# Performance work log

Measured on AMD Instinct MI355X. Metric: run time of the kernel, lower is better.

## Reference

```python
import jax, jax.numpy as jnp
import numpy as np

N = 100000      # num nodes
E = 1600000     # num edges (avg degree 16)
H = 128         # hidden_channels
A = 8           # edge_attr_dim
HID = 16        # edge-MLP hidden dim
DELTA_T = 0.1
LN_EPS = 1e-5


def _layer_norm(x, g, b):
    mu = jnp.mean(x, axis=-1, keepdims=True)
    var = jnp.mean((x - mu) ** 2, axis=-1, keepdims=True)
    return (x - mu) * jax.lax.rsqrt(var + LN_EPS) * g + b


def _edge_mlp(ea, w1, b1, w2, b2):
    # [E,A] -> [E,1] -> [E]
    return (jnp.tanh(ea @ w1 + b1) @ w2 + b2).reshape(-1)


def _spmm_diff(vals, row, col, M, n):
    # Sparse matrix S = diag(d) + off, off[col,row] = vals (scatter-add on duplicates),
    # d = segment_sum(vals, col) with zeros replaced by 1.  Returns S @ M.
    d = jax.ops.segment_sum(vals, col, num_segments=n)
    d = d + (d == 0).astype(vals.dtype)
    off = jax.ops.segment_sum(vals[:, None] * M[row], col, num_segments=n)
    return d[:, None] * M + off


def setup_inputs() -> dict:
    key = jax.random.key(0)
    ks = jax.random.split(key, 12)
    def xavier(k, shape):
        lim = float(np.sqrt(6.0 / (shape[0] + shape[1])))
        return jax.random.uniform(k, shape, jnp.float32, -lim, lim)
    return {
        "u": jax.random.normal(ks[0], (N, H), jnp.float32),
        "edge_index": jax.random.randint(ks[1], (2, E), 0, N, jnp.int64),
        "edge_attr": jax.random.normal(ks[2], (E, A), jnp.float32),
        "num_nodes": N,
        "mlpx_w1": xavier(ks[3], (A, HID)), "mlpx_b1": jnp.zeros((HID,), jnp.float32),
        "mlpx_w2": xavier(ks[4], (HID, 1)), "mlpx_b2": jnp.zeros((1,), jnp.float32),
        "mlpz_w1": xavier(ks[5], (A, HID)), "mlpz_b1": jnp.zeros((HID,), jnp.float32),
        "mlpz_w2": xavier(ks[6], (HID, 1)), "mlpz_b2": jnp.zeros((1,), jnp.float32),
        "weight": xavier(ks[7], (H, H)),
        "az_weight": xavier(ks[8], (H, H)),
        "norm1_g": jnp.ones((H,), jnp.float32), "norm1_b": jnp.zeros((H,), jnp.float32),
        "norm2_g": jnp.ones((H,), jnp.float32), "norm2_b": jnp.zeros((H,), jnp.float32),
        "delta_g": jnp.float32(0.5),
    }


def reference(u, edge_index, edge_attr, num_nodes,
              mlpx_w1, mlpx_b1, mlpx_w2, mlpx_b2,
              mlpz_w1, mlpz_b1, mlpz_w2, mlpz_b2,
              weight, az_weight, norm1_g, norm1_b, norm2_g, norm2_b, delta_g):
    row, col = edge_index[0], edge_index[1]
    delta_x = _edge_mlp(edge_attr, mlpx_w1, mlpx_b1, mlpx_w2, mlpx_b2) + 1e-6
    delta_z = _edge_mlp(edge_attr, mlpz_w1, mlpz_b1, mlpz_w2, mlpz_b2) + 1e-6

    uw2 = (u @ weight) ** 2
    first = _spmm_diff(1.0 / delta_x, row, col, uw2, num_nodes)
    first = jax.nn.silu(_layer_norm(first, norm1_g, norm1_b))

    azt = _spmm_diff(delta_z, row, col, u, num_nodes) @ az_weight
    azt = jax.nn.silu(_layer_norm(azt, norm2_g, norm2_b)) + 1e-6

    u_next = u - DELTA_T * (first + delta_g * azt)
    return jnp.clip(u_next, -10.0, 10.0)
```

## Files before the change

kernel.cpp:

```cpp
#include <hip/hip_runtime.h>

#define HH 128
#define LN_EPS 1e-5f

typedef _Float16 f16x8 __attribute__((ext_vector_type(8)));
typedef _Float16 f16x4 __attribute__((ext_vector_type(4)));
typedef float f32x4 __attribute__((ext_vector_type(4)));

__device__ __forceinline__ ushort f2bf(float v) {
    unsigned u = __float_as_uint(v);
    unsigned r = (u + 0x7FFFu + ((u >> 16) & 1u)) >> 16;
    return (ushort)r;
}
__device__ __forceinline__ float bf2f(unsigned lo16) { return __uint_as_float(lo16 << 16); }

__device__ __forceinline__ bool detect_i64(const int* __restrict__ ei) {
    int odd = ei[2 * (threadIdx.x & 63) + 1];
    return __ballot(odd == 0) == ~0ULL;
}

__global__ __launch_bounds__(256) void k_hist_rank(
    const int* __restrict__ ei, int* __restrict__ cnt,
    ushort* __restrict__ rank, int E)
{
    bool f64 = detect_i64(ei);
    int e0 = (blockIdx.x * 256 + threadIdx.x) * 4;
    if (e0 >= E) return;
    int c[4];
    int nv = min(4, E - e0);
    if (f64) {
        if (nv == 4) {
            int4 a = *(const int4*)&ei[2 * ((size_t)E + e0)];
            int4 b = *(const int4*)&ei[2 * ((size_t)E + e0) + 4];
            c[0] = a.x; c[1] = a.z; c[2] = b.x; c[3] = b.z;
        } else {
            for (int i = 0; i < nv; ++i) c[i] = ei[2 * ((size_t)E + e0 + i)];
        }
    } else {
        if (nv == 4) {
            int4 a = *(const int4*)&ei[(size_t)E + e0];
            c[0] = a.x; c[1] = a.y; c[2] = a.z; c[3] = a.w;
        } else {
            for (int i = 0; i < nv; ++i) c[i] = ei[(size_t)E + e0 + i];
        }
    }
    ushort rk[4];
    for (int i = 0; i < nv; ++i) rk[i] = (ushort)atomicAdd(&cnt[c[i]], 1);
    if (nv == 4) {
        *(ushort4*)&rank[e0] = make_ushort4(rk[0], rk[1], rk[2], rk[3]);
    } else {
        for (int i = 0; i < nv; ++i) rank[e0 + i] = rk[i];
    }
}

__global__ __launch_bounds__(256) void k_scan_a(
    const int* __restrict__ cnt, int* __restrict__ off,
    int* __restrict__ bs, int N)
{
    __shared__ int sm[256];
    int tid = threadIdx.x;
    int base = blockIdx.x * 1024 + tid * 4;
    int v0 = base + 0 < N ? cnt[base + 0] : 0;
    int v1 = base + 1 < N ? cnt[base + 1] : 0;
    int v2 = base + 2 < N ? cnt[base + 2] : 0;
    int v3 = base + 3 < N ? cnt[base + 3] : 0;
    int s = v0 + v1 + v2 + v3;
    sm[tid] = s;
    __syncthreads();
    for (int o = 1; o < 256; o <<= 1) {
        int t = (tid >= o) ? sm[tid - o] : 0;
        __syncthreads();
        sm[tid] += t;
        __syncthreads();
    }
    int excl = sm[tid] - s;
    if (tid == 255) bs[blockIdx.x] = sm[tid];
    if (base + 0 < N) off[base + 0] = excl;
    if (base + 1 < N) off[base + 1] = excl + v0;
    if (base + 2 < N) off[base + 2] = excl + v0 + v1;
    if (base + 3 < N) off[base + 3] = excl + v0 + v1 + v2;
}

__global__ __launch_bounds__(256) void k_scan_bc(
    int* __restrict__ off, const int* __restrict__ bs,
    int N, int E, int nb)
{
    __shared__ int sm[256];
    int tid = threadIdx.x;
    int s = tid < nb ? bs[tid] : 0;
    sm[tid] = s;
    __syncthreads();
    for (int o = 1; o < 256; o <<= 1) {
        int t = (tid >= o) ? sm[tid - o] : 0;
        __syncthreads();
        sm[tid] += t;
        __syncthreads();
    }
    int incl = sm[tid];
    __syncthreads();
    sm[tid] = incl - s;
    __syncthreads();
    int i = blockIdx.x * 256 + tid;
    if (i < N) off[i] += sm[i >> 10];
    if (i == 0) off[N] = E;
}

__global__ __launch_bounds__(256) void k_mlp_fill(
    const float* __restrict__ ea,
    const float* __restrict__ xw1, const float* __restrict__ xb1,
    const float* __restrict__ xw2, const float* __restrict__ xb2,
    const float* __restrict__ zw1, const float* __restrict__ zb1,
    const float* __restrict__ zw2, const float* __restrict__ zb2,
    const int* __restrict__ ei, const int* __restrict__ off,
    const ushort* __restrict__ rank, uint2* __restrict__ csr, int E)
{
    bool f64 = detect_i64(ei);
    int lane = threadIdx.x & 63;
    int wid  = threadIdx.x >> 6;
    int lr = lane & 15, lg = lane >> 4;

    f16x8 wxh, wxl, wzh, wzl;
#pragma unroll
    for (int k = 0; k < 8; ++k) {
        float wx = xw1[k * 16 + lr];
        float wz = zw1[k * 16 + lr];
        _Float16 xh = (_Float16)wx, zh = (_Float16)wz;
        _Float16 xl = (_Float16)(wx - (float)xh);
        _Float16 zl = (_Float16)(wz - (float)zh);
        bool zz = (lg != 0);
        wxh[k] = zz ? (_Float16)0.f : xh;
        wxl[k] = zz ? (_Float16)0.f : xl;
        wzh[k] = zz ? (_Float16)0.f : zh;
        wzl[k] = zz ? (_Float16)0.f : zl;
    }
    float b1x[4], b1z[4], w2x[4], w2z[4];
#pragma unroll
    for (int r = 0; r < 4; ++r) {
        int j = lg * 4 + r;
        b1x[r] = xb1[j]; b1z[r] = zb1[j];
        w2x[r] = xw2[j]; w2z[r] = zw2[j];
    }
    float bx2 = xb2[0], bz2 = zb2[0];

    long long base = (long long)blockIdx.x * 256 + wid * 64;
    long long eL = base + lane;
    size_t eld = (size_t)(eL < (long long)E ? eL : (long long)E - 1);
    float4 a0 = *(const float4*)&ea[eld * 8];
    float4 a1 = *(const float4*)&ea[eld * 8 + 4];
    float aa[8] = {a0.x, a0.y, a0.z, a0.w, a1.x, a1.y, a1.z, a1.w};
    f16x8 ah, al;
#pragma unroll
    for (int i = 0; i < 8; ++i) {
        _Float16 h = (_Float16)aa[i];
        ah[i] = h;
        al[i] = (_Float16)(aa[i] - (float)h);
    }
    uint4 avh = *reinterpret_cast<uint4*>(&ah);
    uint4 avl = *reinterpret_cast<uint4*>(&al);

#pragma unroll
    for (int g = 0; g < 4; ++g) {
        int src = g * 16 + lr;
        uint4 bvh, bvl;
        bvh.x = (unsigned)__shfl((int)avh.x, src);
        bvh.y = (unsigned)__shfl((int)avh.y, src);
        bvh.z = (unsigned)__shfl((int)avh.z, src);
        bvh.w = (unsigned)__shfl((int)avh.w, src);
        bvl.x = (unsigned)__shfl((int)avl.x, src);
        bvl.y = (unsigned)__shfl((int)avl.y, src);
        bvl.z = (unsigned)__shfl((int)avl.z, src);
        bvl.w = (unsigned)__shfl((int)avl.w, src);
        if (lg != 0) {
            bvh.x = 0; bvh.y = 0; bvh.z = 0; bvh.w = 0;
            bvl.x = 0; bvl.y = 0; bvl.z = 0; bvl.w = 0;
        }
        f16x8 bh = *reinterpret_cast<f16x8*>(&bvh);
        f16x8 bl = *reinterpret_cast<f16x8*>(&bvl);

        f32x4 dx = (f32x4){0.f, 0.f, 0.f, 0.f};
        f32x4 dz = (f32x4){0.f, 0.f, 0.f, 0.f};
        dx = __builtin_amdgcn_mfma_f32_16x16x32_f16(wxh, bh, dx, 0, 0, 0);
        dx = __builtin_amdgcn_mfma_f32_16x16x32_f16(wxh, bl, dx, 0, 0, 0);
        dx = __builtin_amdgcn_mfma_f32_16x16x32_f16(wxl, bh, dx, 0, 0, 0);
        dz = __builtin_amdgcn_mfma_f32_16x16x32_f16(wzh, bh, dz, 0, 0, 0);
        dz = __builtin_amdgcn_mfma_f32_16x16x32_f16(wzh, bl, dz, 0, 0, 0);
        dz = __builtin_amdgcn_mfma_f32_16x16x32_f16(wzl, bh, dz, 0, 0, 0);

        float sx = 0.f, sz = 0.f;
#pragma unroll
        for (int r = 0; r < 4; ++r) {
            float tx = __expf(2.f * (dx[r] + b1x[r]));
            float tz = __expf(2.f * (dz[r] + b1z[r]));
            sx += __fdividef(tx - 1.f, tx + 1.f) * w2x[r];
            sz += __fdividef(tz - 1.f, tz + 1.f) * w2z[r];
        }
        sx += __shfl_xor(sx, 16); sx += __shfl_xor(sx, 32);
        sz += __shfl_xor(sz, 16); sz += __shfl_xor(sz, 32);

        long long e = base + g * 16 + lane;
        if (lane < 16 && e < (long long)E) {
            int ec = (int)e;
            int r, c;
            if (f64) {
                r = ei[2 * (size_t)ec];
                c = ei[2 * ((size_t)E + ec)];
            } else {
                r = ei[ec];
                c = ei[(size_t)E + ec];
            }
            int p = off[c] + rank[ec];
            unsigned wx = f2bf(1.0f / (sx + bx2 + 1e-6f));
            unsigned wz = f2bf(sz + bz2 + 1e-6f);
            csr[p] = make_uint2((unsigned)r << 9, wx | (wz << 16));
        }
    }
}

#define WPITCH 136
__global__ __launch_bounds__(256) void k_gemm_fused(
    const float* __restrict__ A, const float* __restrict__ W0,
    const float* __restrict__ W1, _Float16* __restrict__ pk, int N)
{
    __shared__ _Float16 wt[256 * WPITCH];

    int tid = threadIdx.x;
    for (int it = 0; it < 8; ++it) {
        int tile = tid + it * 256;
        int k0 = (tile & 31) * 4, n0 = (tile >> 5) * 4;
        const float* src = (n0 < HH) ? W0 : W1;
        int cn = n0 & (HH - 1);
        float4 r0 = *(const float4*)&src[(k0 + 0) * HH + cn];
        float4 r1 = *(const float4*)&src[(k0 + 1) * HH + cn];
        float4 r2 = *(const float4*)&src[(k0 + 2) * HH + cn];
        float4 r3 = *(const float4*)&src[(k0 + 3) * HH + cn];
        const float* rr[4] = {(const float*)&r0, (const float*)&r1,
                              (const float*)&r2, (const float*)&r3};
#pragma unroll
        for (int j = 0; j < 4; ++j) {
            f16x4 v = {( _Float16)rr[0][j], (_Float16)rr[1][j],
                       ( _Float16)rr[2][j], (_Float16)rr[3][j]};
            *(f16x4*)&wt[(n0 + j) * WPITCH + k0] = v;
        }
    }
    __syncthreads();

    int w = tid >> 6, lane = tid & 63;
    int lr = lane & 15, lg = lane >> 4;

    f32x4 acc[2][16];
#pragma unroll
    for (int rt = 0; rt < 2; ++rt)
#pragma unroll
        for (int ct = 0; ct < 16; ++ct)
            acc[rt][ct] = (f32x4){0.f, 0.f, 0.f, 0.f};

    int rbase = blockIdx.x * 128 + w * 32 + lr;
    int ra0 = min(rbase,      N - 1);
    int ra1 = min(rbase + 16, N - 1);

    for (int ks = 0; ks < 4; ++ks) {
        int kofs = ks * 32 + lg * 8;
        f16x8 ufr[2];
#pragma unroll
        for (int rt = 0; rt < 2; ++rt) {
            const float* ap = &A[(size_t)(rt ? ra1 : ra0) * HH + kofs];
            float4 f0 = *(const float4*)ap;
            float4 f1 = *(const float4*)(ap + 4);
            f16x8 fr = {( _Float16)f0.x, (_Float16)f0.y, (_Float16)f0.z, (_Float16)f0.w,
                        ( _Float16)f1.x, (_Float16)f1.y, (_Float16)f1.z, (_Float16)f1.w};
            ufr[rt] = fr;
        }
#pragma unroll
        for (int ct = 0; ct < 16; ++ct) {
            f16x8 wfr = *(const f16x8*)&wt[(ct * 16 + lr) * WPITCH + kofs];
            acc[0][ct] = __builtin_amdgcn_mfma_f32_16x16x32_f16(wfr, ufr[0], acc[0][ct], 0, 0, 0);
            acc[1][ct] = __builtin_amdgcn_mfma_f32_16x16x32_f16(wfr, ufr[1], acc[1][ct], 0, 0, 0);
        }
    }

#pragma unroll
    for (int rt = 0; rt < 2; ++rt) {
        int r = blockIdx.x * 128 + w * 32 + rt * 16 + lr;
        if (r >= N) continue;
#pragma unroll
        for (int ct = 0; ct < 16; ++ct) {
            int c0 = ct * 16 + lg * 4;
            f16x4 o;
#pragma unroll
            for (int reg = 0; reg < 4; ++reg) {
                float v = acc[rt][ct][reg];
                if (ct < 8) v *= v;
                o[reg] = (_Float16)v;
            }
            *(f16x4*)&pk[(size_t)r * 256 + c0] = o;
        }
    }
}

__global__ __launch_bounds__(256) void k_gather(
    const uint2* __restrict__ csr, const int* __restrict__ off,
    const _Float16* __restrict__ pk, const float* __restrict__ u,
    const float* __restrict__ g1, const float* __restrict__ b1,
    const float* __restrict__ g2, const float* __restrict__ b2,
    const float* __restrict__ dgp, float* __restrict__ outp, int N)
{
    int wave = threadIdx.x >> 6, lane = threadIdx.x & 63;
    int node = blockIdx.x * 4 + wave;
    if (node >= N) return;
    int p = off[node], end = off[node + 1];

    const int  he   = lane >> 5;
    const int  sub  = lane & 31;
    const bool is_az = (lane & 16) != 0;
    const unsigned sub16 = (unsigned)sub * 16;
    const char* pkb = (const char*)pk;

    float acc[8];
#pragma unroll
    for (int j = 0; j < 8; ++j) acc[j] = 0.f;
    float dv = 0.f;

    while (p + 3 < end) {
        uint2 mA = csr[p + he];
        uint2 mB = csr[p + 2 + he];
        float wA = bf2f(is_az ? (mA.y >> 16) : (mA.y & 0xffffu));
        float wB = bf2f(is_az ? (mB.y >> 16) : (mB.y & 0xffffu));
        f16x8 qA = *(const f16x8*)(pkb + mA.x + sub16);
        f16x8 qB = *(const f16x8*)(pkb + mB.x + sub16);
#pragma unroll
        for (int j = 0; j < 8; ++j) acc[j] += wA * (float)qA[j];
#pragma unroll
        for (int j = 0; j < 8; ++j) acc[j] += wB * (float)qB[j];
        dv += wA + wB;
        p += 4;
    }
    while (p < end) {
        int idx = p + he;
        bool ok = idx < end;
        uint2 mm = csr[ok ? idx : p];
        float wv = bf2f(is_az ? (mm.y >> 16) : (mm.y & 0xffffu));
        if (!ok) wv = 0.f;
        f16x8 q = *(const f16x8*)(pkb + mm.x + sub16);
#pragma unroll
        for (int j = 0; j < 8; ++j) acc[j] += wv * (float)q[j];
        dv += wv;
        p += 2;
    }

#pragma unroll
    for (int j = 0; j < 8; ++j) acc[j] += __shfl_xor(acc[j], 32);
    dv += __shfl_xor(dv, 32);
    if (dv == 0.f) dv = 1.f;

    f16x8 qc = *(const f16x8*)(pkb + ((unsigned)node << 9) + sub16);
    float x[8];
#pragma unroll
    for (int j = 0; j < 8; ++j) x[j] = dv * (float)qc[j] + acc[j];

    float s = 0.f;
#pragma unroll
    for (int j = 0; j < 8; ++j) s += x[j];
    s += __shfl_xor(s, 1, 16); s += __shfl_xor(s, 2, 16);
    s += __shfl_xor(s, 4, 16); s += __shfl_xor(s, 8, 16);
    float mu = s * (1.f / 128.f);
    float s2 = 0.f;
#pragma unroll
    for (int j = 0; j < 8; ++j) { x[j] -= mu; s2 += x[j] * x[j]; }
    s2 += __shfl_xor(s2, 1, 16); s2 += __shfl_xor(s2, 2, 16);
    s2 += __shfl_xor(s2, 4, 16); s2 += __shfl_xor(s2, 8, 16);
    float rs = rsqrtf(s2 * (1.f / 128.f) + LN_EPS);

    int c8 = (sub & 15) * 8;
    const float* gp = is_az ? g2 : g1;
    const float* bp = is_az ? b2 : b1;
    float4 gv0 = *(const float4*)&gp[c8];
    float4 gv1 = *(const float4*)&gp[c8 + 4];
    float4 bv0 = *(const float4*)&bp[c8];
    float4 bv1 = *(const float4*)&bp[c8 + 4];
    float gA[8] = {gv0.x, gv0.y, gv0.z, gv0.w, gv1.x, gv1.y, gv1.z, gv1.w};
    float bA[8] = {bv0.x, bv0.y, bv0.z, bv0.w, bv1.x, bv1.y, bv1.z, bv1.w};

    float y[8];
#pragma unroll
    for (int j = 0; j < 8; ++j) {
        float v = x[j] * rs * gA[j] + bA[j];
        v = v / (1.f + __expf(-v));
        if (is_az) v += 1e-6f;
        y[j] = v;
    }

    float dg = *dgp;
    float yz[8];
#pragma unroll
    for (int j = 0; j < 8; ++j) yz[j] = __shfl_xor(y[j], 16);

    if (lane < 16) {
        size_t ub = (size_t)node * HH + c8;
        float4 u0 = *(const float4*)&u[ub];
        float4 u1 = *(const float4*)&u[ub + 4];
        float o[8];
        o[0] = u0.x; o[1] = u0.y; o[2] = u0.z; o[3] = u0.w;
        o[4] = u1.x; o[5] = u1.y; o[6] = u1.z; o[7] = u1.w;
#pragma unroll
        for (int j = 0; j < 8; ++j) {
            float v = o[j] - 0.1f * (y[j] + dg * yz[j]);
            o[j] = fminf(fmaxf(v, -10.f), 10.f);
        }
        *(float4*)&outp[ub]     = make_float4(o[0], o[1], o[2], o[3]);
        *(float4*)&outp[ub + 4] = make_float4(o[4], o[5], o[6], o[7]);
    }
}

extern "C" void kernel_launch(void* const* d_in, const int* in_sizes, int n_in,
                              void* d_out, int out_size, void* d_ws, size_t ws_size,
                              hipStream_t stream)
{
    const float* u   = (const float*)d_in[0];
    const int*   ei  = (const int*)d_in[1];
    const float* ea  = (const float*)d_in[2];
    const float* xw1 = (const float*)d_in[4];
    const float* xb1 = (const float*)d_in[5];
    const float* xw2 = (const float*)d_in[6];
    const float* xb2 = (const float*)d_in[7];
    const float* zw1 = (const float*)d_in[8];
    const float* zb1 = (const float*)d_in[9];
    const float* zw2 = (const float*)d_in[10];
    const float* zb2 = (const float*)d_in[11];
    const float* weight = (const float*)d_in[12];
    const float* azw = (const float*)d_in[13];
    const float* n1g = (const float*)d_in[14];
    const float* n1b = (const float*)d_in[15];
    const float* n2g = (const float*)d_in[16];
    const float* n2b = (const float*)d_in[17];
    const float* dgp = (const float*)d_in[18];

    int N = in_sizes[0] / HH;
    int E = in_sizes[2] / 8;

    _Float16* pk  = (_Float16*)d_ws;
    uint2* csr    = (uint2*)(pk + (size_t)N * 256);
    ushort* rank  = (ushort*)(csr + E);
    int* cnt      = (int*)(rank + ((E + 1) & ~1));
    int* off      = cnt + N;
    int* bs       = off + N + 1;

    (void)hipMemsetAsync(cnt, 0, (size_t)N * sizeof(int), stream);

    k_hist_rank<<<(E / 4 + 255) / 256, 256, 0, stream>>>(ei, cnt, rank, E);

    int nb = (N + 1023) / 1024;
    k_scan_a<<<nb, 256, 0, stream>>>(cnt, off, bs, N);
    k_scan_bc<<<(N + 255) / 256, 256, 0, stream>>>(off, bs, N, E, nb);

    k_mlp_fill<<<(E + 255) / 256, 256, 0, stream>>>(
        ea, xw1, xb1, xw2, xb2, zw1, zb1, zw2, zb2, ei, off, rank, csr, E);

    k_gemm_fused<<<(N + 127) / 128, 256, 0, stream>>>(u, weight, azw, pk, N);

    k_gather<<<(N + 3) / 4, 256, 0, stream>>>(
        csr, off, pk, u, n1g, n1b, n2g, n2b, dgp, (float*)d_out, N);
}
```

Baseline: 304.2 us.

## Merge GEMM and edge-MLP fill into one launch; unroll gather by eight

The dense GEMM blocks and the edge-MLP CSR-fill blocks now run as one kernel, split on block index, so the two independent phases overlap on the GPU and one launch is saved. The gather loop also gets an 8-edge unrolled step so more independent loads are in flight per iteration. The cost is that every block of the fused kernel reserves the ~68KB of shared memory the GEMM needs, which may lower occupancy for the fill blocks, and the extra unroll adds register pressure.

```diff
diff --git a/kernel.cpp b/kernel.cpp
--- a/kernel.cpp
+++ b/kernel.cpp
@@ -105,7 +105,10 @@
     if (i == 0) off[N] = E;
 }
 
-__global__ __launch_bounds__(256) void k_mlp_fill(
+#define WPITCH 136
+__global__ __launch_bounds__(256) void k_fat(
+    const float* __restrict__ A, const float* __restrict__ W0,
+    const float* __restrict__ W1, _Float16* __restrict__ pk, int N, int G,
     const float* __restrict__ ea,
     const float* __restrict__ xw1, const float* __restrict__ xb1,
     const float* __restrict__ xw2, const float* __restrict__ xb2,
@@ -114,185 +117,182 @@
     const int* __restrict__ ei, const int* __restrict__ off,
     const ushort* __restrict__ rank, uint2* __restrict__ csr, int E)
 {
-    bool f64 = detect_i64(ei);
-    int lane = threadIdx.x & 63;
-    int wid  = threadIdx.x >> 6;
-    int lr = lane & 15, lg = lane >> 4;
-
-    f16x8 wxh, wxl, wzh, wzl;
-#pragma unroll
-    for (int k = 0; k < 8; ++k) {
-        float wx = xw1[k * 16 + lr];
-        float wz = zw1[k * 16 + lr];
-        _Float16 xh = (_Float16)wx, zh = (_Float16)wz;
-        _Float16 xl = (_Float16)(wx - (float)xh);
-        _Float16 zl = (_Float16)(wz - (float)zh);
-        bool zz = (lg != 0);
-        wxh[k] = zz ? (_Float16)0.f : xh;
-        wxl[k] = zz ? (_Float16)0.f : xl;
-        wzh[k] = zz ? (_Float16)0.f : zh;
-        wzl[k] = zz ? (_Float16)0.f : zl;
-    }
-    float b1x[4], b1z[4], w2x[4], w2z[4];
-#pragma unroll
-    for (int r = 0; r < 4; ++r) {
-        int j = lg * 4 + r;
-        b1x[r] = xb1[j]; b1z[r] = zb1[j];
-        w2x[r] = xw2[j]; w2z[r] = zw2[j];
-    }
-    float bx2 = xb2[0], bz2 = zb2[0];
-
-    long long base = (long long)blockIdx.x * 256 + wid * 64;
-    long long eL = base + lane;
-    size_t eld = (size_t)(eL < (long long)E ? eL : (long long)E - 1);
-    float4 a0 = *(const float4*)&ea[eld * 8];
-    float4 a1 = *(const float4*)&ea[eld * 8 + 4];
-    float aa[8] = {a0.x, a0.y, a0.z, a0.w, a1.x, a1.y, a1.z, a1.w};
-    f16x8 ah, al;
-#pragma unroll
-    for (int i = 0; i < 8; ++i) {
-        _Float16 h = (_Float16)aa[i];
-        ah[i] = h;
-        al[i] = (_Float16)(aa[i] - (float)h);
-    }
-    uint4 avh = *reinterpret_cast<uint4*>(&ah);
-    uint4 avl = *reinterpret_cast<uint4*>(&al);
-
-#pragma unroll
-    for (int g = 0; g < 4; ++g) {
-        int src = g * 16 + lr;
-        uint4 bvh, bvl;
-        bvh.x = (unsigned)__shfl((int)avh.x, src);
-        bvh.y = (unsigned)__shfl((int)avh.y, src);
-        bvh.z = (unsigned)__shfl((int)avh.z, src);
-        bvh.w = (unsigned)__shfl((int)avh.w, src);
-        bvl.x = (unsigned)__shfl((int)avl.x, src);
-        bvl.y = (unsigned)__shfl((int)avl.y, src);
-        bvl.z = (unsigned)__shfl((int)avl.z, src);
-        bvl.w = (unsigned)__shfl((int)avl.w, src);
-        if (lg != 0) {
-            bvh.x = 0; bvh.y = 0; bvh.z = 0; bvh.w = 0;
-            bvl.x = 0; bvl.y = 0; bvl.z = 0; bvl.w = 0;
-        }
-        f16x8 bh = *reinterpret_cast<f16x8*>(&bvh);
-        f16x8 bl = *reinterpret_cast<f16x8*>(&bvl);
-
-        f32x4 dx = (f32x4){0.f, 0.f, 0.f, 0.f};
-        f32x4 dz = (f32x4){0.f, 0.f, 0.f, 0.f};
-        dx = __builtin_amdgcn_mfma_f32_16x16x32_f16(wxh, bh, dx, 0, 0, 0);
-        dx = __builtin_amdgcn_mfma_f32_16x16x32_f16(wxh, bl, dx, 0, 0, 0);
-        dx = __builtin_amdgcn_mfma_f32_16x16x32_f16(wxl, bh, dx, 0, 0, 0);
-        dz = __builtin_amdgcn_mfma_f32_16x16x32_f16(wzh, bh, dz, 0, 0, 0);
-        dz = __builtin_amdgcn_mfma_f32_16x16x32_f16(wzh, bl, dz, 0, 0, 0);
-        dz = __builtin_amdgcn_mfma_f32_16x16x32_f16(wzl, bh, dz, 0, 0, 0);
-
-        float sx = 0.f, sz = 0.f;
+    if ((int)blockIdx.x < G) {
+        __shared__ _Float16 wt[256 * WPITCH];
+        int bid = blockIdx.x;
+        int tid = threadIdx.x;
+        for (int it = 0; it < 8; ++it) {
+            int tile = tid + it * 256;
+            int k0 = (tile & 31) * 4, n0 = (tile >> 5) * 4;
+            const float* src = (n0 < HH) ? W0 : W1;
+            int cn = n0 & (HH - 1);
+            float4 r0 = *(const float4*)&src[(k0 + 0) * HH + cn];
+            float4 r1 = *(const float4*)&src[(k0 + 1) * HH + cn];
+            float4 r2 = *(const float4*)&src[(k0 + 2) * HH + cn];
+            float4 r3 = *(const float4*)&src[(k0 + 3) * HH + cn];
+            const float* rr[4] = {(const float*)&r0, (const float*)&r1,
+                                  (const float*)&r2, (const float*)&r3};
+#pragma unroll
+            for (int j = 0; j < 4; ++j) {
+                f16x4 v = {( _Float16)rr[0][j], (_Float16)rr[1][j],
+                           ( _Float16)rr[2][j], (_Float16)rr[3][j]};
+                *(f16x4*)&wt[(n0 + j) * WPITCH + k0] = v;
+            }
+        }
+        __syncthreads();
+
+        int w = tid >> 6, lane = tid & 63;
+        int lr = lane & 15, lg = lane >> 4;
+
+        f32x4 acc[2][16];
+#pragma unroll
+        for (int rt = 0; rt < 2; ++rt)
+#pragma unroll
+            for (int ct = 0; ct < 16; ++ct)
+                acc[rt][ct] = (f32x4){0.f, 0.f, 0.f, 0.f};
+
+        int rbase = bid * 128 + w * 32 + lr;
+        int ra0 = min(rbase,      N - 1);
+        int ra1 = min(rbase + 16, N - 1);
+
+        for (int ks = 0; ks < 4; ++ks) {
+            int kofs = ks * 32 + lg * 8;
+            f16x8 ufr[2];
+#pragma unroll
+            for (int rt = 0; rt < 2; ++rt) {
+                const float* ap = &A[(size_t)(rt ? ra1 : ra0) * HH + kofs];
+                float4 f0 = *(const float4*)ap;
+                float4 f1 = *(const float4*)(ap + 4);
+                f16x8 fr = {( _Float16)f0.x, (_Float16)f0.y, (_Float16)f0.z, (_Float16)f0.w,
+                            ( _Float16)f1.x, (_Float16)f1.y, (_Float16)f1.z, (_Float16)f1.w};
+                ufr[rt] = fr;
+            }
+#pragma unroll
+            for (int ct = 0; ct < 16; ++ct) {
+                f16x8 wfr = *(const f16x8*)&wt[(ct * 16 + lr) * WPITCH + kofs];
+                acc[0][ct] = __builtin_amdgcn_mfma_f32_16x16x32_f16(wfr, ufr[0], acc[0][ct], 0, 0, 0);
+                acc[1][ct] = __builtin_amdgcn_mfma_f32_16x16x32_f16(wfr, ufr[1], acc[1][ct], 0, 0, 0);
+            }
+        }
+
+#pragma unroll
+        for (int rt = 0; rt < 2; ++rt) {
+            int r = bid * 128 + w * 32 + rt * 16 + lr;
+            if (r >= N) continue;
+#pragma unroll
+            for (int ct = 0; ct < 16; ++ct) {
+                int c0 = ct * 16 + lg * 4;
+                f16x4 o;
+#pragma unroll
+                for (int reg = 0; reg < 4; ++reg) {
+                    float v = acc[rt][ct][reg];
+                    if (ct < 8) v *= v;
+                    o[reg] = (_Float16)v;
+                }
+                *(f16x4*)&pk[(size_t)r * 256 + c0] = o;
+            }
+        }
+    } else {
+        int bid = blockIdx.x - G;
+        bool f64 = detect_i64(ei);
+        int lane = threadIdx.x & 63;
+        int wid  = threadIdx.x >> 6;
+        int lr = lane & 15, lg = lane >> 4;
+
+        f16x8 wxh, wxl, wzh, wzl;
+#pragma unroll
+        for (int k = 0; k < 8; ++k) {
+            float wx = xw1[k * 16 + lr];
+            float wz = zw1[k * 16 + lr];
+            _Float16 xh = (_Float16)wx, zh = (_Float16)wz;
+            _Float16 xl = (_Float16)(wx - (float)xh);
+            _Float16 zl = (_Float16)(wz - (float)zh);
+            bool zz = (lg != 0);
+            wxh[k] = zz ? (_Float16)0.f : xh;
+            wxl[k] = zz ? (_Float16)0.f : xl;
+            wzh[k] = zz ? (_Float16)0.f : zh;
+            wzl[k] = zz ? (_Float16)0.f : zl;
+        }
+        float b1x[4], b1z[4], w2x[4], w2z[4];
 #pragma unroll
         for (int r = 0; r < 4; ++r) {
-            float tx = __expf(2.f * (dx[r] + b1x[r]));
-            float tz = __expf(2.f * (dz[r] + b1z[r]));
-            sx += __fdividef(tx - 1.f, tx + 1.f) * w2x[r];
-            sz += __fdividef(tz - 1.f, tz + 1.f) * w2z[r];
-        }
-        sx += __shfl_xor(sx, 16); sx += __shfl_xor(sx, 32);
-        sz += __shfl_xor(sz, 16); sz += __shfl_xor(sz, 32);
-
-        long long e = base + g * 16 + lane;
-        if (lane < 16 && e < (long long)E) {
-            int ec = (int)e;
-            int r, c;
-            if (f64) {
-                r = ei[2 * (size_t)ec];
-                c = ei[2 * ((size_t)E + ec)];
-            } else {
-                r = ei[ec];
-                c = ei[(size_t)E + ec];
-            }
-            int p = off[c] + rank[ec];
-            unsigned wx = f2bf(1.0f / (sx + bx2 + 1e-6f));
-            unsigned wz = f2bf(sz + bz2 + 1e-6f);
-            csr[p] = make_uint2((unsigned)r << 9, wx | (wz << 16));
-        }
-    }
-}
-
-#define WPITCH 136
-__global__ __launch_bounds__(256) void k_gemm_fused(
-    const float* __restrict__ A, const float* __restrict__ W0,
-    const float* __restrict__ W1, _Float16* __restrict__ pk, int N)
-{
-    __shared__ _Float16 wt[256 * WPITCH];
-
-    int tid = threadIdx.x;
-    for (int it = 0; it < 8; ++it) {
-        int tile = tid + it * 256;
-        int k0 = (tile & 31) * 4, n0 = (tile >> 5) * 4;
-        const float* src = (n0 < HH) ? W0 : W1;
-        int cn = n0 & (HH - 1);
-        float4 r0 = *(const float4*)&src[(k0 + 0) * HH + cn];
-        float4 r1 = *(const float4*)&src[(k0 + 1) * HH + cn];
-        float4 r2 = *(const float4*)&src[(k0 + 2) * HH + cn];
-        float4 r3 = *(const float4*)&src[(k0 + 3) * HH + cn];
-        const float* rr[4] = {(const float*)&r0, (const float*)&r1,
-                              (const float*)&r2, (const float*)&r3};
-#pragma unroll
-        for (int j = 0; j < 4; ++j) {
-            f16x4 v = {( _Float16)rr[0][j], (_Float16)rr[1][j],
-                       ( _Float16)rr[2][j], (_Float16)rr[3][j]};
-            *(f16x4*)&wt[(n0 + j) * WPITCH + k0] = v;
-        }
-    }
-    __syncthreads();
-
-    int w = tid >> 6, lane = tid & 63;
-    int lr = lane & 15, lg = lane >> 4;
-
-    f32x4 acc[2][16];
-#pragma unroll
-    for (int rt = 0; rt < 2; ++rt)
-#pragma unroll
-        for (int ct = 0; ct < 16; ++ct)
-            acc[rt][ct] = (f32x4){0.f, 0.f, 0.f, 0.f};
-
-    int rbase = blockIdx.x * 128 + w * 32 + lr;
-    int ra0 = min(rbase,      N - 1);
-    int ra1 = min(rbase + 16, N - 1);
-
-    for (int ks = 0; ks < 4; ++ks) {
-        int kofs = ks * 32 + lg * 8;
-        f16x8 ufr[2];
-#pragma unroll
-        for (int rt = 0; rt < 2; ++rt) {
-            const float* ap = &A[(size_t)(rt ? ra1 : ra0) * HH + kofs];
-            float4 f0 = *(const float4*)ap;
-            float4 f1 = *(const float4*)(ap + 4);
-            f16x8 fr = {( _Float16)f0.x, (_Float16)f0.y, (_Float16)f0.z, (_Float16)f0.w,
-                        ( _Float16)f1.x, (_Float16)f1.y, (_Float16)f1.z, (_Float16)f1.w};
-            ufr[rt] = fr;
-        }
-#pragma unroll
-        for (int ct = 0; ct < 16; ++ct) {
-            f16x8 wfr = *(const f16x8*)&wt[(ct * 16 + lr) * WPITCH + kofs];
-            acc[0][ct] = __builtin_amdgcn_mfma_f32_16x16x32_f16(wfr, ufr[0], acc[0][ct], 0, 0, 0);
-            acc[1][ct] = __builtin_amdgcn_mfma_f32_16x16x32_f16(wfr, ufr[1], acc[1][ct], 0, 0, 0);
-        }
-    }
-
-#pragma unroll
-    for (int rt = 0; rt < 2; ++rt) {
-        int r = blockIdx.x * 128 + w * 32 + rt * 16 + lr;
-        if (r >= N) continue;
-#pragma unroll
-        for (int ct = 0; ct < 16; ++ct) {
-            int c0 = ct * 16 + lg * 4;
-            f16x4 o;
-#pragma unroll
-            for (int reg = 0; reg < 4; ++reg) {
-                float v = acc[rt][ct][reg];
-                if (ct < 8) v *= v;
-                o[reg] = (_Float16)v;
-            }
-            *(f16x4*)&pk[(size_t)r * 256 + c0] = o;
+            int j = lg * 4 + r;
+            b1x[r] = xb1[j]; b1z[r] = zb1[j];
+            w2x[r] = xw2[j]; w2z[r] = zw2[j];
+        }
+        float bx2 = xb2[0], bz2 = zb2[0];
+
+        long long base = (long long)bid * 256 + wid * 64;
+        long long eL = base + lane;
+        size_t eld = (size_t)(eL < (long long)E ? eL : (long long)E - 1);
+        float4 a0 = *(const float4*)&ea[eld * 8];
+        float4 a1 = *(const float4*)&ea[eld * 8 + 4];
+        float aa[8] = {a0.x, a0.y, a0.z, a0.w, a1.x, a1.y, a1.z, a1.w};
+        f16x8 ah, al;
+#pragma unroll
+        for (int i = 0; i < 8; ++i) {
+            _Float16 h = (_Float16)aa[i];
+            ah[i] = h;
+            al[i] = (_Float16)(aa[i] - (float)h);
+        }
+        uint4 avh = *reinterpret_cast<uint4*>(&ah);
+        uint4 avl = *reinterpret_cast<uint4*>(&al);
+
+#pragma unroll
+        for (int g = 0; g < 4; ++g) {
+            int src = g * 16 + lr;
+            uint4 bvh, bvl;
+            bvh.x = (unsigned)__shfl((int)avh.x, src);
+            bvh.y = (unsigned)__shfl((int)avh.y, src);
+            bvh.z = (unsigned)__shfl((int)avh.z, src);
+            bvh.w = (unsigned)__shfl((int)avh.w, src);
+            bvl.x = (unsigned)__shfl((int)avl.x, src);
+            bvl.y = (unsigned)__shfl((int)avl.y, src);
+            bvl.z = (unsigned)__shfl((int)avl.z, src);
+            bvl.w = (unsigned)__shfl((int)avl.w, src);
+            if (lg != 0) {
+                bvh.x = 0; bvh.y = 0; bvh.z = 0; bvh.w = 0;
+                bvl.x = 0; bvl.y = 0; bvl.z = 0; bvl.w = 0;
+            }
+            f16x8 bh = *reinterpret_cast<f16x8*>(&bvh);
+            f16x8 bl = *reinterpret_cast<f16x8*>(&bvl);
+
+            f32x4 dx = (f32x4){0.f, 0.f, 0.f, 0.f};
+            f32x4 dz = (f32x4){0.f, 0.f, 0.f, 0.f};
+            dx = __builtin_amdgcn_mfma_f32_16x16x32_f16(wxh, bh, dx, 0, 0, 0);
+            dx = __builtin_amdgcn_mfma_f32_16x16x32_f16(wxh, bl, dx, 0, 0, 0);
+            dx = __builtin_amdgcn_mfma_f32_16x16x32_f16(wxl, bh, dx, 0, 0, 0);
+            dz = __builtin_amdgcn_mfma_f32_16x16x32_f16(wzh, bh, dz, 0, 0, 0);
+            dz = __builtin_amdgcn_mfma_f32_16x16x32_f16(wzh, bl, dz, 0, 0, 0);
+            dz = __builtin_amdgcn_mfma_f32_16x16x32_f16(wzl, bh, dz, 0, 0, 0);
+
+            float sx = 0.f, sz = 0.f;
+#pragma unroll
+            for (int r = 0; r < 4; ++r) {
+                float tx = __expf(2.f * (dx[r] + b1x[r]));
+                float tz = __expf(2.f * (dz[r] + b1z[r]));
+                sx += __fdividef(tx - 1.f, tx + 1.f) * w2x[r];
+                sz += __fdividef(tz - 1.f, tz + 1.f) * w2z[r];
+            }
+            sx += __shfl_xor(sx, 16); sx += __shfl_xor(sx, 32);
+            sz += __shfl_xor(sz, 16); sz += __shfl_xor(sz, 32);
+
+            long long e = base + g * 16 + lane;
+            if (lane < 16 && e < (long long)E) {
+                int ec = (int)e;
+                int r, c;
+                if (f64) {
+                    r = ei[2 * (size_t)ec];
+                    c = ei[2 * ((size_t)E + ec)];
+                } else {
+                    r = ei[ec];
+                    c = ei[(size_t)E + ec];
+                }
+                int p = off[c] + rank[ec];
+                unsigned wx = f2bf(1.0f / (sx + bx2 + 1e-6f));
+                unsigned wz = f2bf(sz + bz2 + 1e-6f);
+                csr[p] = make_uint2((unsigned)r << 9, wx | (wz << 16));
+            }
         }
     }
 }
@@ -320,6 +320,30 @@
     for (int j = 0; j < 8; ++j) acc[j] = 0.f;
     float dv = 0.f;
 
+    while (p + 7 < end) {
+        uint2 m0 = csr[p + he];
+        uint2 m1 = csr[p + 2 + he];
+        uint2 m2 = csr[p + 4 + he];
+        uint2 m3 = csr[p + 6 + he];
+        float w0 = bf2f(is_az ? (m0.y >> 16) : (m0.y & 0xffffu));
+        float w1 = bf2f(is_az ? (m1.y >> 16) : (m1.y & 0xffffu));
+        float w2 = bf2f(is_az ? (m2.y >> 16) : (m2.y & 0xffffu));
+        float w3 = bf2f(is_az ? (m3.y >> 16) : (m3.y & 0xffffu));
+        f16x8 q0 = *(const f16x8*)(pkb + m0.x + sub16);
+        f16x8 q1 = *(const f16x8*)(pkb + m1.x + sub16);
+        f16x8 q2 = *(const f16x8*)(pkb + m2.x + sub16);
+        f16x8 q3 = *(const f16x8*)(pkb + m3.x + sub16);
+#pragma unroll
+        for (int j = 0; j < 8; ++j) acc[j] += w0 * (float)q0[j];
+#pragma unroll
+        for (int j = 0; j < 8; ++j) acc[j] += w1 * (float)q1[j];
+#pragma unroll
+        for (int j = 0; j < 8; ++j) acc[j] += w2 * (float)q2[j];
+#pragma unroll
+        for (int j = 0; j < 8; ++j) acc[j] += w3 * (float)q3[j];
+        dv += (w0 + w1) + (w2 + w3);
+        p += 8;
+    }
     while (p + 3 < end) {
         uint2 mA = csr[p + he];
         uint2 mB = csr[p + 2 + he];
@@ -452,10 +476,12 @@
     k_scan_a<<<nb, 256, 0, stream>>>(cnt, off, bs, N);
     k_scan_bc<<<(N + 255) / 256, 256, 0, stream>>>(off, bs, N, E, nb);
 
-    k_mlp_fill<<<(E + 255) / 256, 256, 0, stream>>>(
-        ea, xw1, xb1, xw2, xb2, zw1, zb1, zw2, zb2, ei, off, rank, csr, E);
-
-    k_gemm_fused<<<(N + 127) / 128, 256, 0, stream>>>(u, weight, azw, pk, N);
+    int G = (N + 127) / 128;
+    int F = (E + 255) / 256;
+    k_fat<<<G + F, 256, 0, stream>>>(
+        u, weight, azw, pk, N, G,
+        ea, xw1, xb1, xw2, xb2, zw1, zb1, zw2, zb2,
+        ei, off, rank, csr, E);
 
     k_gather<<<(N + 3) / 4, 256, 0, stream>>>(
         csr, off, pk, u, n1g, n1b, n2g, n2b, dgp, (float*)d_out, N);
```

Result: slower. 349.0 us (+14.7%).
